# Optimization experiments

Hardware: AMD Instinct MI355X
Metric: run time of the kernel (lower is better)

## Reference

```python
import jax, jax.numpy as jnp
import numpy as np

LN_EPS = 1e-5
SUM_CLAMP = 1e-12


def setup_inputs() -> dict:
    key = jax.random.key(0)
    ks = jax.random.split(key, 10)
    L, D, H, P, E = 200000, 512, 512, 16384, 200000
    lesion_x = jax.random.normal(ks[0], (L, D), dtype=jnp.float32)
    edge_index = jnp.stack([
        jax.random.randint(ks[1], (E,), 0, P),   # patient idx
        jax.random.randint(ks[2], (E,), 0, L),   # lesion idx
    ], axis=0).astype(jnp.int64)
    s1 = 1.0 / np.sqrt(D)
    s2 = 1.0 / np.sqrt(H)
    W1 = jax.random.uniform(ks[3], (H, D), jnp.float32, -s1, s1)
    b1 = jax.random.uniform(ks[4], (H,), jnp.float32, -s1, s1)
    W2 = jax.random.uniform(ks[5], (1, H), jnp.float32, -s2, s2)
    b2 = jax.random.uniform(ks[6], (1,), jnp.float32, -s2, s2)
    Wp = jax.random.uniform(ks[7], (768, D), jnp.float32, -s1, s1)
    bp = jax.random.uniform(ks[8], (768,), jnp.float32, -s1, s1)
    gamma = jnp.ones((768,), jnp.float32)
    beta = jnp.zeros((768,), jnp.float32)
    return dict(lesion_x=lesion_x, patient_to_lesion_edge_index=edge_index,
                num_patients_in_batch=P, W1=W1, b1=b1, W2=W2, b2=b2,
                Wp=Wp, bp=bp, gamma=gamma, beta=beta)


def reference(lesion_x, patient_to_lesion_edge_index, num_patients_in_batch,
              W1, b1, W2, b2, Wp, bp, gamma, beta):
    P = int(num_patients_in_batch)
    pat = patient_to_lesion_edge_index[0]
    les = patient_to_lesion_edge_index[1]
    feats = lesion_x[les]                                  # [E, D] gather
    h = jnp.tanh(feats @ W1.T + b1)                        # [E, H]
    scores = (h @ W2.T + b2)[:, 0]                         # [E]
    smax = jax.ops.segment_max(scores, pat, num_segments=P)  # [P]
    ex = jnp.exp(scores - smax[pat])                       # [E]
    esum = jax.ops.segment_sum(ex, pat, num_segments=P)
    esum = jnp.maximum(esum, SUM_CLAMP)
    alpha = ex / esum[pat]                                 # [E]
    agg = jax.ops.segment_sum(feats * alpha[:, None], pat, num_segments=P)  # [P, D]
    proj = agg @ Wp.T + bp                                 # [P, 768]
    mu = jnp.mean(proj, axis=-1, keepdims=True)
    var = jnp.mean(jnp.square(proj - mu), axis=-1, keepdims=True)
    out = (proj - mu) * jax.lax.rsqrt(var + LN_EPS) * gamma + beta
    return out
```

## Files before the change

### kernel.cpp

```cpp
#include <hip/hip_runtime.h>
#include <hip/hip_bf16.h>

#define D_DIM 512
#define H_DIM 512
#define O_DIM 768

using bf16x8 = __attribute__((ext_vector_type(8))) short;
using f32x4  = __attribute__((ext_vector_type(4))) float;

static __device__ __forceinline__ unsigned short f2bf(float f){
  unsigned u = __float_as_uint(f);
  u += 0x7fffu + ((u >> 16) & 1u);
  return (unsigned short)(u >> 16);
}

static __device__ __forceinline__ float fast_tanh(float x){
  float e = __expf(2.f * x);
  return 1.f - 2.f / (e + 1.f);
}

static __device__ __forceinline__ unsigned f2ord(float f){
  unsigned u = __float_as_uint(f);
  return (u & 0x80000000u) ? ~u : (u | 0x80000000u);
}
static __device__ __forceinline__ float ord2f(unsigned u){
  u = (u & 0x80000000u) ? (u & 0x7fffffffu) : ~u;
  return __uint_as_float(u);
}

static __device__ __forceinline__ void gload16(const void* g, void* l){
  __builtin_amdgcn_global_load_lds(
      (const __attribute__((address_space(1))) void*)g,
      (__attribute__((address_space(3))) void*)l, 16, 0, 0);
}

__global__ void cvt_bf16(const float* __restrict__ in,
                         unsigned short* __restrict__ out, int n8)
{
  int stride = gridDim.x * blockDim.x;
  for (int i = blockIdx.x*blockDim.x + threadIdx.x; i < n8; i += stride){
    const float4* p = (const float4*)in + (size_t)i*2;
    float4 a = p[0], b = p[1];
    union { unsigned short us[8]; uint4 u4; } pk;
    pk.us[0]=f2bf(a.x); pk.us[1]=f2bf(a.y); pk.us[2]=f2bf(a.z); pk.us[3]=f2bf(a.w);
    pk.us[4]=f2bf(b.x); pk.us[5]=f2bf(b.y); pk.us[6]=f2bf(b.z); pk.us[7]=f2bf(b.w);
    ((uint4*)out)[i] = pk.u4;
  }
}

template<int MODE>
__launch_bounds__(256, 2)
__global__ void gemm_bf16(const short* __restrict__ A,
                          const short* __restrict__ Bm,
                          const float* __restrict__ bias,
                          const float* __restrict__ w2,
                          float* __restrict__ out,
                          int M, int outStride)
{
  __shared__ short lds_a[128*64];
  __shared__ short lds_b[128*64];

  const int tid  = threadIdx.x;
  const int lane = tid & 63;
  const int w    = tid >> 6;
  const int wr   = w >> 1, wc = w & 1;
  const int lr   = lane & 15;
  const int lk   = lane >> 4;

  const int colBase = blockIdx.x * 128;
  const int rowBase = blockIdx.y * 128;

  f32x4 acc[4][4];
  #pragma unroll
  for (int i = 0; i < 4; ++i)
    #pragma unroll
    for (int j = 0; j < 4; ++j)
      acc[i][j] = (f32x4){0.f, 0.f, 0.f, 0.f};

  const int subrow = lane >> 3;
  const int gpre   = lane & 7;

  for (int kt = 0; kt < 512/64; ++kt){
    const int kOff = kt * 64;
    #pragma unroll
    for (int c = 0; c < 4; ++c){
      int r    = w*32 + c*8 + subrow;
      int gran = gpre ^ (r & 7);
      int gA   = rowBase + r; if (gA > M-1) gA = M-1;
      gload16(A  + (size_t)gA*512 + kOff + gran*8, &lds_a[(w*32 + c*8)*64]);
      int gB   = colBase + r;
      gload16(Bm + (size_t)gB*512 + kOff + gran*8, &lds_b[(w*32 + c*8)*64]);
    }
    __syncthreads();
    #pragma unroll
    for (int kk = 0; kk < 2; ++kk){
      bf16x8 af[4], bfr[4];
      #pragma unroll
      for (int mf = 0; mf < 4; ++mf){
        int r   = wr*64 + mf*16 + lr;
        int idx = (r*64 + kk*32 + lk*8) ^ ((r & 7) << 3);
        af[mf] = *(bf16x8*)&lds_a[idx];
      }
      #pragma unroll
      for (int nf = 0; nf < 4; ++nf){
        int r   = wc*64 + nf*16 + lr;
        int idx = (r*64 + kk*32 + lk*8) ^ ((r & 7) << 3);
        bfr[nf] = *(bf16x8*)&lds_b[idx];
      }
      #pragma unroll
      for (int mf = 0; mf < 4; ++mf)
        #pragma unroll
        for (int nf = 0; nf < 4; ++nf)
          acc[mf][nf] = __builtin_amdgcn_mfma_f32_16x16x32_bf16(
              af[mf], bfr[nf], acc[mf][nf], 0, 0, 0);
    }
    __syncthreads();
  }

  if (MODE == 0){
    #pragma unroll
    for (int mf = 0; mf < 4; ++mf){
      float part[4] = {0.f,0.f,0.f,0.f};
      #pragma unroll
      for (int nf = 0; nf < 4; ++nf){
        int gc = colBase + wc*64 + nf*16 + lr;
        float b = bias[gc], wv = w2[gc];
        #pragma unroll
        for (int r = 0; r < 4; ++r)
          part[r] += fast_tanh(acc[mf][nf][r] + b) * wv;
      }
      #pragma unroll
      for (int r = 0; r < 4; ++r){
        part[r] += __shfl_xor(part[r], 1);
        part[r] += __shfl_xor(part[r], 2);
        part[r] += __shfl_xor(part[r], 4);
        part[r] += __shfl_xor(part[r], 8);
      }
      if (lr == 0){
        int gr = rowBase + wr*64 + mf*16 + lk*4;
        #pragma unroll
        for (int r = 0; r < 4; ++r)
          if (gr + r < M) atomicAdd(&out[gr + r], part[r]);
      }
    }
  } else {
    #pragma unroll
    for (int mf = 0; mf < 4; ++mf){
      int gr = rowBase + wr*64 + mf*16 + lk*4;
      #pragma unroll
      for (int nf = 0; nf < 4; ++nf){
        int gc = colBase + wc*64 + nf*16 + lr;
        float b = bias[gc];
        #pragma unroll
        for (int r = 0; r < 4; ++r)
          if (gr + r < M) out[(size_t)(gr + r)*outStride + gc] = acc[mf][nf][r] + b;
      }
    }
  }
}

template<int MODE>
__launch_bounds__(256, 2)
__global__ void gemm_conv(const float* __restrict__ A,
                          const float* __restrict__ Bm,
                          const float* __restrict__ bias,
                          const float* __restrict__ w2,
                          float* __restrict__ out,
                          int M, int outStride)
{
  __shared__ short lds_a[128*64];
  __shared__ short lds_b[128*64];

  const int tid  = threadIdx.x;
  const int lane = tid & 63;
  const int w    = tid >> 6;
  const int wr   = w >> 1, wc = w & 1;
  const int lr   = lane & 15;
  const int lk   = lane >> 4;
  const int rowBase = blockIdx.y * 128;
  const int colBase = blockIdx.x * 128;

  f32x4 acc[4][4];
  #pragma unroll
  for (int i = 0; i < 4; ++i)
    #pragma unroll
    for (int j = 0; j < 4; ++j)
      acc[i][j] = (f32x4){0.f, 0.f, 0.f, 0.f};

  for (int kt = 0; kt < 512/64; ++kt){
    const int kOff = kt * 64;
    #pragma unroll
    for (int it = 0; it < 8; ++it){
      int i   = tid + it*256;
      int row = i >> 4, c4 = i & 15;
      int idx = (row*64 + c4*4) ^ ((row & 7) << 3);
      float4 va = {0.f,0.f,0.f,0.f};
      int gRow = rowBase + row;
      if (gRow < M) va = *(const float4*)(A + (size_t)gRow*512 + kOff + c4*4);
      uint2 pa = { (unsigned)f2bf(va.x) | ((unsigned)f2bf(va.y) << 16),
                   (unsigned)f2bf(va.z) | ((unsigned)f2bf(va.w) << 16) };
      *(uint2*)&lds_a[idx] = pa;
      int gN = colBase + row;
      float4 vb = *(const float4*)(Bm + (size_t)gN*512 + kOff + c4*4);
      uint2 pb = { (unsigned)f2bf(vb.x) | ((unsigned)f2bf(vb.y) << 16),
                   (unsigned)f2bf(vb.z) | ((unsigned)f2bf(vb.w) << 16) };
      *(uint2*)&lds_b[idx] = pb;
    }
    __syncthreads();
    #pragma unroll
    for (int kk = 0; kk < 2; ++kk){
      bf16x8 af[4], bfr[4];
      #pragma unroll
      for (int mf = 0; mf < 4; ++mf){
        int r   = wr*64 + mf*16 + lr;
        int idx = (r*64 + kk*32 + lk*8) ^ ((r & 7) << 3);
        af[mf] = *(bf16x8*)&lds_a[idx];
      }
      #pragma unroll
      for (int nf = 0; nf < 4; ++nf){
        int r   = wc*64 + nf*16 + lr;
        int idx = (r*64 + kk*32 + lk*8) ^ ((r & 7) << 3);
        bfr[nf] = *(bf16x8*)&lds_b[idx];
      }
      #pragma unroll
      for (int mf = 0; mf < 4; ++mf)
        #pragma unroll
        for (int nf = 0; nf < 4; ++nf)
          acc[mf][nf] = __builtin_amdgcn_mfma_f32_16x16x32_bf16(
              af[mf], bfr[nf], acc[mf][nf], 0, 0, 0);
    }
    __syncthreads();
  }

  if (MODE == 0){
    #pragma unroll
    for (int mf = 0; mf < 4; ++mf){
      float part[4] = {0.f,0.f,0.f,0.f};
      #pragma unroll
      for (int nf = 0; nf < 4; ++nf){
        int gc = colBase + wc*64 + nf*16 + lr;
        float b = bias[gc], wv = w2[gc];
        #pragma unroll
        for (int r = 0; r < 4; ++r)
          part[r] += fast_tanh(acc[mf][nf][r] + b) * wv;
      }
      #pragma unroll
      for (int r = 0; r < 4; ++r){
        part[r] += __shfl_xor(part[r], 1);
        part[r] += __shfl_xor(part[r], 2);
        part[r] += __shfl_xor(part[r], 4);
        part[r] += __shfl_xor(part[r], 8);
      }
      if (lr == 0){
        int gr = rowBase + wr*64 + mf*16 + lk*4;
        #pragma unroll
        for (int r = 0; r < 4; ++r)
          if (gr + r < M) atomicAdd(&out[gr + r], part[r]);
      }
    }
  } else {
    #pragma unroll
    for (int mf = 0; mf < 4; ++mf){
      int gr = rowBase + wr*64 + mf*16 + lk*4;
      #pragma unroll
      for (int nf = 0; nf < 4; ++nf){
        int gc = colBase + wc*64 + nf*16 + lr;
        float b = bias[gc];
        #pragma unroll
        for (int r = 0; r < 4; ++r)
          if (gr + r < M) out[(size_t)(gr + r)*outStride + gc] = acc[mf][nf][r] + b;
      }
    }
  }
}

__global__ void edge_pass1(const int* __restrict__ edge, int E,
                           const float* __restrict__ scores,
                           unsigned* __restrict__ smax_o,
                           int* __restrict__ hist)
{
  int e = blockIdx.x*256 + threadIdx.x;
  if (e >= E) return;
  int p = edge[e], l = edge[E + e];
  atomicMax(&smax_o[p], f2ord(scores[l]));
  atomicAdd(&hist[p], 1);
}

__global__ void scan_kernel(const int* __restrict__ hist,
                            int* __restrict__ offsets, int P)
{
  __shared__ int s[1024];
  int t = threadIdx.x;
  int local[16]; int sum = 0;
  #pragma unroll
  for (int i = 0; i < 16; ++i){
    int idx = t*16 + i;
    local[i] = (idx < P) ? hist[idx] : 0;
    sum += local[i];
  }
  s[t] = sum;
  __syncthreads();
  for (int off = 1; off < 1024; off <<= 1){
    int v = (t >= off) ? s[t - off] : 0;
    __syncthreads();
    s[t] += v;
    __syncthreads();
  }
  int run = s[t] - sum;
  #pragma unroll
  for (int i = 0; i < 16; ++i){
    int idx = t*16 + i;
    if (idx < P) offsets[idx] = run;
    run += local[i];
  }
}

__global__ void edge_pass2(const int* __restrict__ edge, int E,
                           const float* __restrict__ scores,
                           const unsigned* __restrict__ smax_o,
                           float* __restrict__ ex,
                           float* __restrict__ esum,
                           const int* __restrict__ offsets,
                           int* __restrict__ cursor,
                           int* __restrict__ sorted)
{
  int e = blockIdx.x*256 + threadIdx.x;
  if (e >= E) return;
  int p = edge[e], l = edge[E + e];
  float v = __expf(scores[l] - ord2f(smax_o[p]));
  ex[e] = v;
  atomicAdd(&esum[p], v);
  int pos = atomicAdd(&cursor[p], 1);
  sorted[offsets[p] + pos] = e;
}

template<bool BF>
__global__ void agg_kernel(const int* __restrict__ edge, int E,
                           const float* __restrict__ lesion_x,
                           const float* __restrict__ ex,
                           const float* __restrict__ esum,
                           const int* __restrict__ offsets,
                           const int* __restrict__ hist,
                           const int* __restrict__ sorted,
                           float* __restrict__ aggf,
                           unsigned* __restrict__ aggb)
{
  int p = blockIdx.x;
  int n = hist[p];
  if (n == 0) return;
  int start = offsets[p];
  float inv = 1.f / fmaxf(esum[p], 1e-12f);
  int t = threadIdx.x;
  float a0 = 0.f, a1 = 0.f;
  for (int i = 0; i < n; ++i){
    int e = sorted[start + i];
    int l = edge[E + e];
    float alpha = ex[e] * inv;
    float2 f = *(const float2*)(lesion_x + (size_t)l*512 + t*2);
    a0 += alpha * f.x;
    a1 += alpha * f.y;
  }
  if (BF){
    aggb[(size_t)p*256 + t] = (unsigned)f2bf(a0) | ((unsigned)f2bf(a1) << 16);
  } else {
    aggf[(size_t)p*512 + t*2]     = a0;
    aggf[(size_t)p*512 + t*2 + 1] = a1;
  }
}

__global__ void ln_kernel(float* __restrict__ out,
                          const float* __restrict__ gamma,
                          const float* __restrict__ beta)
{
  __shared__ float red1[4];
  __shared__ float red2[4];
  int p = blockIdx.x;
  float* row = out + (size_t)p*768;
  int t = threadIdx.x;
  float v0 = row[t], v1 = row[t+256], v2 = row[t+512];
  float s = v0 + v1 + v2;
  #pragma unroll
  for (int off = 32; off; off >>= 1) s += __shfl_down(s, off);
  int lane = t & 63, wv = t >> 6;
  if (lane == 0) red1[wv] = s;
  __syncthreads();
  float mean = (red1[0]+red1[1]+red1[2]+red1[3]) * (1.f/768.f);
  float d0 = v0-mean, d1 = v1-mean, d2 = v2-mean;
  float q = d0*d0 + d1*d1 + d2*d2;
  #pragma unroll
  for (int off = 32; off; off >>= 1) q += __shfl_down(q, off);
  if (lane == 0) red2[wv] = q;
  __syncthreads();
  float var = (red2[0]+red2[1]+red2[2]+red2[3]) * (1.f/768.f);
  float inv = rsqrtf(var + 1e-5f);
  row[t]     = d0*inv*gamma[t]     + beta[t];
  row[t+256] = d1*inv*gamma[t+256] + beta[t+256];
  row[t+512] = d2*inv*gamma[t+512] + beta[t+512];
}

extern "C" void kernel_launch(void* const* d_in, const int* in_sizes, int n_in,
                              void* d_out, int out_size, void* d_ws, size_t ws_size,
                              hipStream_t stream)
{
  const float* lesion_x = (const float*)d_in[0];
  const int*   edge     = (const int*)d_in[1];
  const float* W1    = (const float*)d_in[3];
  const float* b1    = (const float*)d_in[4];
  const float* W2    = (const float*)d_in[5];
  const float* Wp    = (const float*)d_in[7];
  const float* bp    = (const float*)d_in[8];
  const float* gamma = (const float*)d_in[9];
  const float* beta  = (const float*)d_in[10];

  const int L = in_sizes[0] / D_DIM;
  const int E = in_sizes[1] / 2;
  const int P = out_size / O_DIM;

  auto al = [](size_t x){ return (x + 255) & ~(size_t)255; };
  char* ws = (char*)d_ws;
  size_t oScores = 0;
  size_t oSmax   = oScores + al((size_t)L*4);
  size_t oEsum   = oSmax   + al((size_t)P*4);
  size_t oHist   = oEsum   + al((size_t)P*4);
  size_t oCursor = oHist   + al((size_t)P*4);
  size_t smallEnd= oCursor + al((size_t)P*4);
  size_t oAggB   = smallEnd;
  size_t oAggF   = oAggB   + al((size_t)P*D_DIM*2);
  size_t oOff    = oAggF   + al((size_t)P*D_DIM*4);
  size_t oEx     = oOff    + al((size_t)P*4);
  size_t oSorted = oEx     + al((size_t)E*4);
  size_t oAb     = oSorted + al((size_t)E*4);
  size_t oW1b    = oAb     + al((size_t)L*D_DIM*2);
  size_t oWpb    = oW1b    + al((size_t)H_DIM*D_DIM*2);
  size_t need    = oWpb    + al((size_t)O_DIM*D_DIM*2);

  float*    scores = (float*)(ws + oScores);
  unsigned* smax_o = (unsigned*)(ws + oSmax);
  float*    esum   = (float*)(ws + oEsum);
  int*      hist   = (int*)(ws + oHist);
  int*      cursor = (int*)(ws + oCursor);
  unsigned* aggb   = (unsigned*)(ws + oAggB);
  float*    aggf   = (float*)(ws + oAggF);
  int*      offs   = (int*)(ws + oOff);
  float*    ex     = (float*)(ws + oEx);
  int*      sorted = (int*)(ws + oSorted);
  short*    Ab     = (short*)(ws + oAb);
  short*    W1b    = (short*)(ws + oW1b);
  short*    Wpb    = (short*)(ws + oWpb);

  const bool big = (ws_size >= need);

  hipMemsetAsync(d_ws, 0, smallEnd, stream);
  dim3 b256(256);
  int eb = (E + 255) / 256;

  if (big){
    hipMemsetAsync(ws + oAggB, 0, (size_t)P*D_DIM*2, stream);
    cvt_bf16<<<2048, b256, 0, stream>>>(lesion_x, (unsigned short*)Ab, L*D_DIM/8);
    cvt_bf16<<<128,  b256, 0, stream>>>(W1, (unsigned short*)W1b, H_DIM*D_DIM/8);
    cvt_bf16<<<192,  b256, 0, stream>>>(Wp, (unsigned short*)Wpb, O_DIM*D_DIM/8);
    gemm_bf16<0><<<dim3(H_DIM/128, (L + 127)/128), b256, 0, stream>>>(
        Ab, W1b, b1, W2, scores, L, 0);
    edge_pass1<<<eb, b256, 0, stream>>>(edge, E, scores, smax_o, hist);
    scan_kernel<<<1, 1024, 0, stream>>>(hist, offs, P);
    edge_pass2<<<eb, b256, 0, stream>>>(edge, E, scores, smax_o, ex, esum,
                                        offs, cursor, sorted);
    agg_kernel<true><<<P, b256, 0, stream>>>(edge, E, lesion_x, ex, esum, offs,
                                             hist, sorted, nullptr, aggb);
    gemm_bf16<1><<<dim3(O_DIM/128, P/128), b256, 0, stream>>>(
        (const short*)aggb, Wpb, bp, nullptr, (float*)d_out, P, O_DIM);
  } else {
    hipMemsetAsync(ws + oAggF, 0, (size_t)P*D_DIM*4, stream);
    gemm_conv<0><<<dim3(H_DIM/128, (L + 127)/128), b256, 0, stream>>>(
        lesion_x, W1, b1, W2, scores, L, 0);
    edge_pass1<<<eb, b256, 0, stream>>>(edge, E, scores, smax_o, hist);
    scan_kernel<<<1, 1024, 0, stream>>>(hist, offs, P);
    edge_pass2<<<eb, b256, 0, stream>>>(edge, E, scores, smax_o, ex, esum,
                                        offs, cursor, sorted);
    agg_kernel<false><<<P, b256, 0, stream>>>(edge, E, lesion_x, ex, esum, offs,
                                              hist, sorted, aggf, nullptr);
    gemm_conv<1><<<dim3(O_DIM/128, P/128), b256, 0, stream>>>(
        aggf, Wp, bp, nullptr, (float*)d_out, P, O_DIM);
  }
  ln_kernel<<<P, b256, 0, stream>>>((float*)d_out, gamma, beta);
}
```

Baseline: 514.2 us.

## Fuse lesion bf16 conversion into score GEMM via fp32 LDS staging

Removes the separate pass that converts all of lesion_x to bf16. The first GEMM now streams fp32 rows directly into LDS with global_load_lds and converts them to bf16 while building MFMA fragments, using the hardware packed-convert instruction. Workgroups are remapped so consecutive tiles land on the same XCD, which is meant to improve L2 reuse of A rows across the four column tiles. This saves a large read and write of a 200k x 512 temporary, but doubles LDS traffic for the A tile and adds conversion work inside the inner loop. The fallback fp32 path is removed.

```diff
diff --git a/kernel.cpp b/kernel.cpp
--- a/kernel.cpp
+++ b/kernel.cpp
@@ -12,6 +12,12 @@
   unsigned u = __float_as_uint(f);
   u += 0x7fffu + ((u >> 16) & 1u);
   return (unsigned short)(u >> 16);
+}
+
+static __device__ __forceinline__ unsigned cvtpk(float lo, float hi){
+  unsigned r;
+  asm("v_cvt_pk_bf16_f32 %0, %1, %2" : "=v"(r) : "v"(lo), "v"(hi));
+  return r;
 }
 
 static __device__ __forceinline__ float fast_tanh(float x){
@@ -48,14 +54,127 @@
   }
 }
 
-template<int MODE>
 __launch_bounds__(256, 2)
-__global__ void gemm_bf16(const short* __restrict__ A,
-                          const short* __restrict__ Bm,
-                          const float* __restrict__ bias,
-                          const float* __restrict__ w2,
-                          float* __restrict__ out,
-                          int M, int outStride)
+__global__ void gemm1_f32a(const float* __restrict__ A,
+                           const short* __restrict__ Bm,
+                           const float* __restrict__ bias,
+                           const float* __restrict__ w2,
+                           float* __restrict__ out,
+                           int M, int nwg)
+{
+  __shared__ float lds_af[128*64];
+  __shared__ short lds_b [128*64];
+
+  {
+  }
+  const int q  = nwg >> 3, rr = nwg & 7;
+  const int xcd = blockIdx.x & 7, bidx = blockIdx.x >> 3;
+  const int swz = (xcd < rr ? xcd*(q+1) : rr*(q+1) + (xcd-rr)*q) + bidx;
+  const int colBase = (swz & 3) * 128;
+  const int rowBase = (swz >> 2) * 128;
+
+  const int tid  = threadIdx.x;
+  const int lane = tid & 63;
+  const int w    = tid >> 6;
+  const int wr   = w >> 1, wc = w & 1;
+  const int lr   = lane & 15;
+  const int lk   = lane >> 4;
+
+  f32x4 acc[4][4];
+  #pragma unroll
+  for (int i = 0; i < 4; ++i)
+    #pragma unroll
+    for (int j = 0; j < 4; ++j)
+      acc[i][j] = (f32x4){0.f, 0.f, 0.f, 0.f};
+
+  const int rlocA = lane >> 4;
+  const int jA    = lane & 15;
+  const int rlocB = lane >> 3;
+  const int jB    = lane & 7;
+
+  for (int kt = 0; kt < 512/64; ++kt){
+    const int kOff = kt * 64;
+    #pragma unroll
+    for (int c = 0; c < 8; ++c){
+      int rt = w*32 + c*4 + rlocA;
+      int gA = rowBase + rt; if (gA > M-1) gA = M-1;
+      int js = jA ^ (rt & 7);
+      gload16(A + (size_t)gA*512 + kOff + js*4, &lds_af[(w*32 + c*4)*64]);
+    }
+    #pragma unroll
+    for (int c = 0; c < 4; ++c){
+      int rt = w*32 + c*8 + rlocB;
+      int gB = colBase + rt;
+      int js = jB ^ (rt & 7);
+      gload16(Bm + (size_t)gB*512 + kOff + js*8, &lds_b[(w*32 + c*8)*64]);
+    }
+    __syncthreads();
+    #pragma unroll
+    for (int kk = 0; kk < 2; ++kk){
+      bf16x8 af[4], bfr[4];
+      #pragma unroll
+      for (int mf = 0; mf < 4; ++mf){
+        int r   = wr*64 + mf*16 + lr;
+        int rx  = r & 7;
+        int g0  = kk*8 + lk*2;
+        float4 lo4 = *(const float4*)&lds_af[r*64 + ((g0     ^ rx) << 2)];
+        float4 hi4 = *(const float4*)&lds_af[r*64 + (((g0+1) ^ rx) << 2)];
+        union { bf16x8 v; unsigned u[4]; } fa;
+        fa.u[0] = cvtpk(lo4.x, lo4.y);
+        fa.u[1] = cvtpk(lo4.z, lo4.w);
+        fa.u[2] = cvtpk(hi4.x, hi4.y);
+        fa.u[3] = cvtpk(hi4.z, hi4.w);
+        af[mf] = fa.v;
+      }
+      #pragma unroll
+      for (int nf = 0; nf < 4; ++nf){
+        int r   = wc*64 + nf*16 + lr;
+        int idx = (r*64 + kk*32 + lk*8) ^ ((r & 7) << 3);
+        bfr[nf] = *(bf16x8*)&lds_b[idx];
+      }
+      #pragma unroll
+      for (int mf = 0; mf < 4; ++mf)
+        #pragma unroll
+        for (int nf = 0; nf < 4; ++nf)
+          acc[mf][nf] = __builtin_amdgcn_mfma_f32_16x16x32_bf16(
+              af[mf], bfr[nf], acc[mf][nf], 0, 0, 0);
+    }
+    __syncthreads();
+  }
+
+  #pragma unroll
+  for (int mf = 0; mf < 4; ++mf){
+    float part[4] = {0.f,0.f,0.f,0.f};
+    #pragma unroll
+    for (int nf = 0; nf < 4; ++nf){
+      int gc = colBase + wc*64 + nf*16 + lr;
+      float b = bias[gc], wv = w2[gc];
+      #pragma unroll
+      for (int r = 0; r < 4; ++r)
+        part[r] += fast_tanh(acc[mf][nf][r] + b) * wv;
+    }
+    #pragma unroll
+    for (int r = 0; r < 4; ++r){
+      part[r] += __shfl_xor(part[r], 1);
+      part[r] += __shfl_xor(part[r], 2);
+      part[r] += __shfl_xor(part[r], 4);
+      part[r] += __shfl_xor(part[r], 8);
+    }
+    if (lr == 0){
+      int gr = rowBase + wr*64 + mf*16 + lk*4;
+      #pragma unroll
+      for (int r = 0; r < 4; ++r)
+        if (gr + r < M) atomicAdd(&out[gr + r], part[r]);
+    }
+  }
+}
+
+__launch_bounds__(256, 2)
+__global__ void gemm2_bf16(const short* __restrict__ A,
+                           const short* __restrict__ Bm,
+                           const float* __restrict__ bias,
+                           float* __restrict__ out,
+                           int M, int outStride)
 {
   __shared__ short lds_a[128*64];
   __shared__ short lds_b[128*64];
@@ -117,159 +236,16 @@
     __syncthreads();
   }
 
-  if (MODE == 0){
-    #pragma unroll
-    for (int mf = 0; mf < 4; ++mf){
-      float part[4] = {0.f,0.f,0.f,0.f};
-      #pragma unroll
-      for (int nf = 0; nf < 4; ++nf){
-        int gc = colBase + wc*64 + nf*16 + lr;
-        float b = bias[gc], wv = w2[gc];
-        #pragma unroll
-        for (int r = 0; r < 4; ++r)
-          part[r] += fast_tanh(acc[mf][nf][r] + b) * wv;
-      }
-      #pragma unroll
-      for (int r = 0; r < 4; ++r){
-        part[r] += __shfl_xor(part[r], 1);
-        part[r] += __shfl_xor(part[r], 2);
-        part[r] += __shfl_xor(part[r], 4);
-        part[r] += __shfl_xor(part[r], 8);
-      }
-      if (lr == 0){
-        int gr = rowBase + wr*64 + mf*16 + lk*4;
-        #pragma unroll
-        for (int r = 0; r < 4; ++r)
-          if (gr + r < M) atomicAdd(&out[gr + r], part[r]);
-      }
-    }
-  } else {
-    #pragma unroll
-    for (int mf = 0; mf < 4; ++mf){
-      int gr = rowBase + wr*64 + mf*16 + lk*4;
-      #pragma unroll
-      for (int nf = 0; nf < 4; ++nf){
-        int gc = colBase + wc*64 + nf*16 + lr;
-        float b = bias[gc];
-        #pragma unroll
-        for (int r = 0; r < 4; ++r)
-          if (gr + r < M) out[(size_t)(gr + r)*outStride + gc] = acc[mf][nf][r] + b;
-      }
-    }
-  }
-}
-
-template<int MODE>
-__launch_bounds__(256, 2)
-__global__ void gemm_conv(const float* __restrict__ A,
-                          const float* __restrict__ Bm,
-                          const float* __restrict__ bias,
-                          const float* __restrict__ w2,
-                          float* __restrict__ out,
-                          int M, int outStride)
-{
-  __shared__ short lds_a[128*64];
-  __shared__ short lds_b[128*64];
-
-  const int tid  = threadIdx.x;
-  const int lane = tid & 63;
-  const int w    = tid >> 6;
-  const int wr   = w >> 1, wc = w & 1;
-  const int lr   = lane & 15;
-  const int lk   = lane >> 4;
-  const int rowBase = blockIdx.y * 128;
-  const int colBase = blockIdx.x * 128;
-
-  f32x4 acc[4][4];
-  #pragma unroll
-  for (int i = 0; i < 4; ++i)
-    #pragma unroll
-    for (int j = 0; j < 4; ++j)
-      acc[i][j] = (f32x4){0.f, 0.f, 0.f, 0.f};
-
-  for (int kt = 0; kt < 512/64; ++kt){
-    const int kOff = kt * 64;
-    #pragma unroll
-    for (int it = 0; it < 8; ++it){
-      int i   = tid + it*256;
-      int row = i >> 4, c4 = i & 15;
-      int idx = (row*64 + c4*4) ^ ((row & 7) << 3);
-      float4 va = {0.f,0.f,0.f,0.f};
-      int gRow = rowBase + row;
-      if (gRow < M) va = *(const float4*)(A + (size_t)gRow*512 + kOff + c4*4);
-      uint2 pa = { (unsigned)f2bf(va.x) | ((unsigned)f2bf(va.y) << 16),
-                   (unsigned)f2bf(va.z) | ((unsigned)f2bf(va.w) << 16) };
-      *(uint2*)&lds_a[idx] = pa;
-      int gN = colBase + row;
-      float4 vb = *(const float4*)(Bm + (size_t)gN*512 + kOff + c4*4);
-      uint2 pb = { (unsigned)f2bf(vb.x) | ((unsigned)f2bf(vb.y) << 16),
-                   (unsigned)f2bf(vb.z) | ((unsigned)f2bf(vb.w) << 16) };
-      *(uint2*)&lds_b[idx] = pb;
-    }
-    __syncthreads();
-    #pragma unroll
-    for (int kk = 0; kk < 2; ++kk){
-      bf16x8 af[4], bfr[4];
-      #pragma unroll
-      for (int mf = 0; mf < 4; ++mf){
-        int r   = wr*64 + mf*16 + lr;
-        int idx = (r*64 + kk*32 + lk*8) ^ ((r & 7) << 3);
-        af[mf] = *(bf16x8*)&lds_a[idx];
-      }
-      #pragma unroll
-      for (int nf = 0; nf < 4; ++nf){
-        int r   = wc*64 + nf*16 + lr;
-        int idx = (r*64 + kk*32 + lk*8) ^ ((r & 7) << 3);
-        bfr[nf] = *(bf16x8*)&lds_b[idx];
-      }
-      #pragma unroll
-      for (int mf = 0; mf < 4; ++mf)
-        #pragma unroll
-        for (int nf = 0; nf < 4; ++nf)
-          acc[mf][nf] = __builtin_amdgcn_mfma_f32_16x16x32_bf16(
-              af[mf], bfr[nf], acc[mf][nf], 0, 0, 0);
-    }
-    __syncthreads();
-  }
-
-  if (MODE == 0){
-    #pragma unroll
-    for (int mf = 0; mf < 4; ++mf){
-      float part[4] = {0.f,0.f,0.f,0.f};
-      #pragma unroll
-      for (int nf = 0; nf < 4; ++nf){
-        int gc = colBase + wc*64 + nf*16 + lr;
-        float b = bias[gc], wv = w2[gc];
-        #pragma unroll
-        for (int r = 0; r < 4; ++r)
-          part[r] += fast_tanh(acc[mf][nf][r] + b) * wv;
-      }
-      #pragma unroll
-      for (int r = 0; r < 4; ++r){
-        part[r] += __shfl_xor(part[r], 1);
-        part[r] += __shfl_xor(part[r], 2);
-        part[r] += __shfl_xor(part[r], 4);
-        part[r] += __shfl_xor(part[r], 8);
-      }
-      if (lr == 0){
-        int gr = rowBase + wr*64 + mf*16 + lk*4;
-        #pragma unroll
-        for (int r = 0; r < 4; ++r)
-          if (gr + r < M) atomicAdd(&out[gr + r], part[r]);
-      }
-    }
-  } else {
-    #pragma unroll
-    for (int mf = 0; mf < 4; ++mf){
-      int gr = rowBase + wr*64 + mf*16 + lk*4;
-      #pragma unroll
-      for (int nf = 0; nf < 4; ++nf){
-        int gc = colBase + wc*64 + nf*16 + lr;
-        float b = bias[gc];
-        #pragma unroll
-        for (int r = 0; r < 4; ++r)
-          if (gr + r < M) out[(size_t)(gr + r)*outStride + gc] = acc[mf][nf][r] + b;
-      }
+  #pragma unroll
+  for (int mf = 0; mf < 4; ++mf){
+    int gr = rowBase + wr*64 + mf*16 + lk*4;
+    #pragma unroll
+    for (int nf = 0; nf < 4; ++nf){
+      int gc = colBase + wc*64 + nf*16 + lr;
+      float b = bias[gc];
+      #pragma unroll
+      for (int r = 0; r < 4; ++r)
+        if (gr + r < M) out[(size_t)(gr + r)*outStride + gc] = acc[mf][nf][r] + b;
     }
   }
 }
@@ -334,7 +310,6 @@
   sorted[offsets[p] + pos] = e;
 }
 
-template<bool BF>
 __global__ void agg_kernel(const int* __restrict__ edge, int E,
                            const float* __restrict__ lesion_x,
                            const float* __restrict__ ex,
@@ -342,7 +317,6 @@
                            const int* __restrict__ offsets,
                            const int* __restrict__ hist,
                            const int* __restrict__ sorted,
-                           float* __restrict__ aggf,
                            unsigned* __restrict__ aggb)
 {
   int p = blockIdx.x;
@@ -360,12 +334,7 @@
     a0 += alpha * f.x;
     a1 += alpha * f.y;
   }
-  if (BF){
-    aggb[(size_t)p*256 + t] = (unsigned)f2bf(a0) | ((unsigned)f2bf(a1) << 16);
-  } else {
-    aggf[(size_t)p*512 + t*2]     = a0;
-    aggf[(size_t)p*512 + t*2 + 1] = a1;
-  }
+  aggb[(size_t)p*256 + t] = cvtpk(a0, a1);
 }
 
 __global__ void ln_kernel(float* __restrict__ out,
@@ -425,14 +394,14 @@
   size_t oCursor = oHist   + al((size_t)P*4);
   size_t smallEnd= oCursor + al((size_t)P*4);
   size_t oAggB   = smallEnd;
-  size_t oAggF   = oAggB   + al((size_t)P*D_DIM*2);
-  size_t oOff    = oAggF   + al((size_t)P*D_DIM*4);
+  size_t aggEnd  = oAggB   + al((size_t)P*D_DIM*2);
+  size_t oOff    = aggEnd;
   size_t oEx     = oOff    + al((size_t)P*4);
   size_t oSorted = oEx     + al((size_t)E*4);
-  size_t oAb     = oSorted + al((size_t)E*4);
-  size_t oW1b    = oAb     + al((size_t)L*D_DIM*2);
+  size_t oW1b    = oSorted + al((size_t)E*4);
   size_t oWpb    = oW1b    + al((size_t)H_DIM*D_DIM*2);
   size_t need    = oWpb    + al((size_t)O_DIM*D_DIM*2);
+  (void)need;
 
   float*    scores = (float*)(ws + oScores);
   unsigned* smax_o = (unsigned*)(ws + oSmax);
@@ -440,47 +409,32 @@
   int*      hist   = (int*)(ws + oHist);
   int*      cursor = (int*)(ws + oCursor);
   unsigned* aggb   = (unsigned*)(ws + oAggB);
-  float*    aggf   = (float*)(ws + oAggF);
   int*      offs   = (int*)(ws + oOff);
   float*    ex     = (float*)(ws + oEx);
   int*      sorted = (int*)(ws + oSorted);
-  short*    Ab     = (short*)(ws + oAb);
   short*    W1b    = (short*)(ws + oW1b);
   short*    Wpb    = (short*)(ws + oWpb);
 
-  const bool big = (ws_size >= need);
-
   hipMemsetAsync(d_ws, 0, smallEnd, stream);
+  hipMemsetAsync(ws + oAggB, 0, (size_t)P*D_DIM*2, stream);
+
   dim3 b256(256);
   int eb = (E + 255) / 256;
 
-  if (big){
-    hipMemsetAsync(ws + oAggB, 0, (size_t)P*D_DIM*2, stream);
-    cvt_bf16<<<2048, b256, 0, stream>>>(lesion_x, (unsigned short*)Ab, L*D_DIM/8);
-    cvt_bf16<<<128,  b256, 0, stream>>>(W1, (unsigned short*)W1b, H_DIM*D_DIM/8);
-    cvt_bf16<<<192,  b256, 0, stream>>>(Wp, (unsigned short*)Wpb, O_DIM*D_DIM/8);
-    gemm_bf16<0><<<dim3(H_DIM/128, (L + 127)/128), b256, 0, stream>>>(
-        Ab, W1b, b1, W2, scores, L, 0);
-    edge_pass1<<<eb, b256, 0, stream>>>(edge, E, scores, smax_o, hist);
-    scan_kernel<<<1, 1024, 0, stream>>>(hist, offs, P);
-    edge_pass2<<<eb, b256, 0, stream>>>(edge, E, scores, smax_o, ex, esum,
-                                        offs, cursor, sorted);
-    agg_kernel<true><<<P, b256, 0, stream>>>(edge, E, lesion_x, ex, esum, offs,
-                                             hist, sorted, nullptr, aggb);
-    gemm_bf16<1><<<dim3(O_DIM/128, P/128), b256, 0, stream>>>(
-        (const short*)aggb, Wpb, bp, nullptr, (float*)d_out, P, O_DIM);
-  } else {
-    hipMemsetAsync(ws + oAggF, 0, (size_t)P*D_DIM*4, stream);
-    gemm_conv<0><<<dim3(H_DIM/128, (L + 127)/128), b256, 0, stream>>>(
-        lesion_x, W1, b1, W2, scores, L, 0);
-    edge_pass1<<<eb, b256, 0, stream>>>(edge, E, scores, smax_o, hist);
-    scan_kernel<<<1, 1024, 0, stream>>>(hist, offs, P);
-    edge_pass2<<<eb, b256, 0, stream>>>(edge, E, scores, smax_o, ex, esum,
-                                        offs, cursor, sorted);
-    agg_kernel<false><<<P, b256, 0, stream>>>(edge, E, lesion_x, ex, esum, offs,
-                                              hist, sorted, aggf, nullptr);
-    gemm_conv<1><<<dim3(O_DIM/128, P/128), b256, 0, stream>>>(
-        aggf, Wp, bp, nullptr, (float*)d_out, P, O_DIM);
-  }
+  cvt_bf16<<<128, b256, 0, stream>>>(W1, (unsigned short*)W1b, H_DIM*D_DIM/8);
+  cvt_bf16<<<192, b256, 0, stream>>>(Wp, (unsigned short*)Wpb, O_DIM*D_DIM/8);
+
+  int nRow = (L + 127) / 128;
+  int nwg  = 4 * nRow;
+  gemm1_f32a<<<nwg, b256, 0, stream>>>(lesion_x, W1b, b1, W2, scores, L, nwg);
+
+  edge_pass1<<<eb, b256, 0, stream>>>(edge, E, scores, smax_o, hist);
+  scan_kernel<<<1, 1024, 0, stream>>>(hist, offs, P);
+  edge_pass2<<<eb, b256, 0, stream>>>(edge, E, scores, smax_o, ex, esum,
+                                      offs, cursor, sorted);
+  agg_kernel<<<P, b256, 0, stream>>>(edge, E, lesion_x, ex, esum, offs,
+                                     hist, sorted, aggb);
+  gemm2_bf16<<<dim3(O_DIM/128, P/128), b256, 0, stream>>>(
+      (const short*)aggb, Wpb, bp, (float*)d_out, P, O_DIM);
   ln_kernel<<<P, b256, 0, stream>>>((float*)d_out, gamma, beta);
 }
```

After: 430.0 us. 16.4% less time.
